# Optimization experiments

Hardware: AMD Instinct MI355X
Metric: run time of the kernel (lower is better)

Reference implementation:

```python
import jax, jax.numpy as jnp
import numpy as np

N_NODES = 2000
N_EDGES = 40000
DILATION = 2
DC = 32  # dilation_channels
C_IN = 32  # in_channels (= gcn out_channels)


def setup_inputs() -> dict:
    key = jax.random.key(0)
    ks = jax.random.split(key, 8)
    x = jax.random.normal(ks[0], (4, 34, N_NODES, C_IN), jnp.float32)
    edge_index = jax.random.randint(ks[1], (2, N_EDGES), 0, N_NODES, dtype=jnp.int64)
    edge_weight = jax.random.uniform(ks[2], (N_EDGES,), jnp.float32)
    gate1_w = jax.random.normal(ks[3], (DC, C_IN, 1, 2), jnp.float32) * 0.1
    gate1_b = jnp.zeros((DC,), jnp.float32)
    gate2_w = jax.random.normal(ks[4], (DC, C_IN, 1, 2), jnp.float32) * 0.1
    gate2_b = jnp.zeros((DC,), jnp.float32)
    gcn_w = jax.random.normal(ks[5], (DC, C_IN), jnp.float32) * 0.1
    gcn_b = jnp.zeros((C_IN,), jnp.float32)
    return {"x": x, "edge_index": edge_index, "edge_weight": edge_weight,
            "gate1_w": gate1_w, "gate1_b": gate1_b,
            "gate2_w": gate2_w, "gate2_b": gate2_b,
            "gcn_w": gcn_w, "gcn_b": gcn_b}


def _gate_conv(x_nchw, w, b):
    # Conv2d(kernel=(1,2), dilation=DILATION), VALID padding -> acts on time (W) axis
    y = jax.lax.conv_general_dilated(
        x_nchw, w, window_strides=(1, 1), padding='VALID',
        rhs_dilation=(1, DILATION),
        dimension_numbers=('NCHW', 'OIHW', 'NCHW'))
    return y + b[None, :, None, None]


def reference(x, edge_index, edge_weight, gate1_w, gate1_b, gate2_w, gate2_b, gcn_w, gcn_b):
    B, T, N, C = x.shape
    xt = jnp.transpose(x, (0, 3, 2, 1))  # (B, C, N, T)
    g1 = jnp.tanh(_gate_conv(xt, gate1_w, gate1_b))      # (B, DC, N, T')
    g2 = jax.nn.sigmoid(_gate_conv(xt, gate2_w, gate2_b))
    g = g1 * g2
    Tp = g.shape[-1]
    h = jnp.transpose(g, (0, 3, 2, 1)).reshape(B * Tp, N, DC)  # (Bt, N, DC)

    # GCN normalization with self loops (PyG gcn_norm, add_self_loops=True)
    row, col = edge_index[0], edge_index[1]
    loop = jnp.arange(N, dtype=edge_index.dtype)
    row_f = jnp.concatenate([row, loop])
    col_f = jnp.concatenate([col, loop])
    w_f = jnp.concatenate([edge_weight, jnp.ones((N,), edge_weight.dtype)])
    deg = jax.ops.segment_sum(w_f, col_f, num_segments=N)
    dis = jnp.where(deg > 0, jax.lax.rsqrt(deg), 0.0)
    norm = dis[row_f] * w_f * dis[col_f]  # (E+N,)

    hw = jnp.einsum('bnd,de->bne', h, gcn_w)          # (Bt, N, C_IN)
    msgs = hw[:, row_f, :] * norm[None, :, None]      # (Bt, E+N, C_IN)
    out = jnp.zeros_like(hw).at[:, col_f, :].add(msgs) + gcn_b  # scatter over targets

    return out.reshape(B, Tp, N, C_IN)  # (B, T', N, in_channels)
```

## Files before the change

### kernel.cpp

```cpp
#include <hip/hip_runtime.h>
#include <hip/hip_bf16.h>

typedef short short8 __attribute__((ext_vector_type(8)));
typedef float floatx4 __attribute__((ext_vector_type(4)));
typedef unsigned short ushort8_t __attribute__((ext_vector_type(8)));

#define NN 2000
#define NE 40000
#define NB 4
#define T_IN 34
#define TP 32
#define NBT (NB * TP)
#define NPOS (NB * TP * NN)
#define CAP 96


__device__ inline unsigned short f2bf(float x) {
    unsigned int u = __float_as_uint(x);
    u = u + 0x7fff + ((u >> 16) & 1);
    return (unsigned short)(u >> 16);
}
__device__ inline void splitPair(float x0, float x1, unsigned& hi, unsigned& lo) {
    unsigned u0 = __float_as_uint(x0), u1 = __float_as_uint(x1);
    hi = __builtin_amdgcn_perm(u1, u0, 0x07060302u);
    float r0 = x0 - __uint_as_float(u0 & 0xffff0000u);
    float r1 = x1 - __uint_as_float(u1 & 0xffff0000u);
    lo = __builtin_amdgcn_perm(__float_as_uint(r1), __float_as_uint(r0), 0x07060302u);
}
__device__ inline void splitA8(const float* v, short8& hi, short8& lo) {
    union { unsigned u[4]; short8 s; } H, L;
#pragma unroll
    for (int j = 0; j < 4; ++j) {
        unsigned h_, l_;
        splitPair(v[2 * j], v[2 * j + 1], h_, l_);
        H.u[j] = h_; L.u[j] = l_;
    }
    hi = H.s; lo = L.s;
}

__global__ __launch_bounds__(256) void conv_deg_kernel(
        const float* __restrict__ x,
        const float* __restrict__ w1, const float* __restrict__ b1,
        const float* __restrict__ w2, const float* __restrict__ b2,
        unsigned short* __restrict__ h2,
        const int* __restrict__ row, const int* __restrict__ col,
        const float* __restrict__ ew,
        float* __restrict__ deg, int* __restrict__ cursor,
        int2* __restrict__ pcsr) {
    if (blockIdx.x >= 1000) {
        int e = (blockIdx.x - 1000) * 256 + threadIdx.x;
        if (e < NE) {
            int c = col[e], r = row[e];
            float w = ew[e];
            atomicAdd(&deg[c], w);
            int slot = atomicAdd(&cursor[c], 1);
            if (slot < CAP) pcsr[c * CAP + slot] = make_int2(r, __float_as_int(w));
        }
        return;
    }

    int l = threadIdx.x & 63;
    int w = threadIdx.x >> 6;
    int colL = l & 15, q = l >> 4;

    short8 Whi[2][2][2], Wlo[2][2][2];
#pragma unroll
    for (int g = 0; g < 2; ++g) {
        const float* wp = g ? w2 : w1;
#pragma unroll
        for (int d = 0; d < 2; ++d)
#pragma unroll
        for (int tap = 0; tap < 2; ++tap) {
            float wv[8];
#pragma unroll
            for (int j = 0; j < 8; ++j)
                wv[j] = wp[(d * 16 + colL) * 64 + (q * 8 + j) * 2 + tap];
            splitA8(wv, Whi[g][d][tap], Wlo[g][d][tap]);
        }
    }
    float bias[2][2] = { { b1[colL], b1[colL + 16] }, { b2[colL], b2[colL + 16] } };

    for (int i = 0; i < 4; ++i) {
        int tile = blockIdx.x * 16 + w * 4 + i;
        int pos0 = tile * 16;
        int bt = pos0 / 2000;
        int n0 = pos0 - bt * 2000;
        int b_ = bt >> 5, t_ = bt & 31;
        const float* xa = x + (((b_ * T_IN + t_) * NN) + n0 + colL) * 32 + q * 8;
        const float* xb = xa + 2 * NN * 32;
        float va[8], vb[8];
        *(float4*)va       = *(const float4*)xa;
        *(float4*)(va + 4) = *(const float4*)(xa + 4);
        *(float4*)vb       = *(const float4*)xb;
        *(float4*)(vb + 4) = *(const float4*)(xb + 4);
        short8 Ahi0, Alo0, Ahi1, Alo1;
        splitA8(va, Ahi0, Alo0);
        splitA8(vb, Ahi1, Alo1);

        floatx4 acc[2][2];
#pragma unroll
        for (int g = 0; g < 2; ++g)
#pragma unroll
        for (int d = 0; d < 2; ++d) {
            float bv = bias[g][d];
            floatx4 a = { bv, bv, bv, bv };
            a = __builtin_amdgcn_mfma_f32_16x16x32_bf16(Ahi0, Whi[g][d][0], a, 0, 0, 0);
            a = __builtin_amdgcn_mfma_f32_16x16x32_bf16(Ahi1, Whi[g][d][1], a, 0, 0, 0);
            a = __builtin_amdgcn_mfma_f32_16x16x32_bf16(Alo0, Whi[g][d][0], a, 0, 0, 0);
            a = __builtin_amdgcn_mfma_f32_16x16x32_bf16(Alo1, Whi[g][d][1], a, 0, 0, 0);
            a = __builtin_amdgcn_mfma_f32_16x16x32_bf16(Ahi0, Wlo[g][d][0], a, 0, 0, 0);
            a = __builtin_amdgcn_mfma_f32_16x16x32_bf16(Ahi1, Wlo[g][d][1], a, 0, 0, 0);
            acc[g][d] = a;
        }

#pragma unroll
        for (int d = 0; d < 2; ++d)
#pragma unroll
        for (int r = 0; r < 4; ++r) {
            float g1 = acc[0][d][r];
            float g2 = acc[1][d][r];
            float e2 = __expf(2.0f * g1);
            float th = (e2 - 1.0f) / (e2 + 1.0f);
            float sg = 1.0f / (1.0f + __expf(-g2));
            float h = th * sg;
            int n = n0 + q * 4 + r;
            h2[(n * NBT + bt) * 32 + d * 16 + colL] = f2bf(h);
        }
    }
}

__device__ inline void acc8(float2* a2, const ushort8_t& v, float nr) {
    union { ushort8_t s; unsigned u[4]; } U; U.s = v;
#pragma unroll
    for (int j = 0; j < 4; ++j) {
        float2 vv;
        vv.x = __uint_as_float(U.u[j] << 16);
        vv.y = __uint_as_float(U.u[j] & 0xffff0000u);
        a2[j].x += vv.x * nr;
        a2[j].y += vv.y * nr;
    }
}

__global__ __launch_bounds__(256) void agg_gcn_kernel(
        const unsigned short* __restrict__ h2,
        const float* __restrict__ deg, const int* __restrict__ cursor,
        const int2* __restrict__ pcsr,
        const float* __restrict__ gw, const float* __restrict__ gb,
        float* __restrict__ out) {
    __shared__ float st[64 * 36];
    int l = threadIdx.x & 63;
    int wv = threadIdx.x >> 6;
    int b = blockIdx.x;
    int cp = b & 7;
    int n = (b >> 3) * 4 + wv;
    int colL = l & 15, q = l >> 4;

    short8 Bhi[2], Blo[2];
#pragma unroll
    for (int d = 0; d < 2; ++d) {
        float wv8[8];
#pragma unroll
        for (int j = 0; j < 8; ++j)
            wv8[j] = gw[(q * 8 + j) * 32 + d * 16 + colL];
        splitA8(wv8, Bhi[d], Blo[d]);
    }
    float gb0 = gb[colL], gb1 = gb[colL + 16];

    const unsigned short* base = h2 + cp * 512 + l * 8;
    float dn = rsqrtf(deg[n] + 1.0f);
    float w0 = dn * dn;
    float2 a2[4] = { {0,0}, {0,0}, {0,0}, {0,0} };
    {
        ushort8_t sv = *(const ushort8_t*)(base + (size_t)n * 4096);
        acc8(a2, sv, w0);
    }
    int cnt = cursor[n]; if (cnt > CAP) cnt = CAP;
    const int2* slots = pcsr + n * CAP;
    int i = 0;
    for (; i + 8 <= cnt; i += 8) {
        int2 e0 = slots[i],     e1 = slots[i + 1], e2 = slots[i + 2], e3 = slots[i + 3];
        int2 e4 = slots[i + 4], e5 = slots[i + 5], e6 = slots[i + 6], e7 = slots[i + 7];
        float n0 = rsqrtf(deg[e0.x] + 1.0f) * __int_as_float(e0.y) * dn;
        float n1 = rsqrtf(deg[e1.x] + 1.0f) * __int_as_float(e1.y) * dn;
        float n2 = rsqrtf(deg[e2.x] + 1.0f) * __int_as_float(e2.y) * dn;
        float n3 = rsqrtf(deg[e3.x] + 1.0f) * __int_as_float(e3.y) * dn;
        float n4 = rsqrtf(deg[e4.x] + 1.0f) * __int_as_float(e4.y) * dn;
        float n5 = rsqrtf(deg[e5.x] + 1.0f) * __int_as_float(e5.y) * dn;
        float n6 = rsqrtf(deg[e6.x] + 1.0f) * __int_as_float(e6.y) * dn;
        float n7 = rsqrtf(deg[e7.x] + 1.0f) * __int_as_float(e7.y) * dn;
        ushort8_t v0 = *(const ushort8_t*)(base + (size_t)e0.x * 4096);
        ushort8_t v1 = *(const ushort8_t*)(base + (size_t)e1.x * 4096);
        ushort8_t v2 = *(const ushort8_t*)(base + (size_t)e2.x * 4096);
        ushort8_t v3 = *(const ushort8_t*)(base + (size_t)e3.x * 4096);
        ushort8_t v4 = *(const ushort8_t*)(base + (size_t)e4.x * 4096);
        ushort8_t v5 = *(const ushort8_t*)(base + (size_t)e5.x * 4096);
        ushort8_t v6 = *(const ushort8_t*)(base + (size_t)e6.x * 4096);
        ushort8_t v7 = *(const ushort8_t*)(base + (size_t)e7.x * 4096);
        acc8(a2, v0, n0); acc8(a2, v1, n1); acc8(a2, v2, n2); acc8(a2, v3, n3);
        acc8(a2, v4, n4); acc8(a2, v5, n5); acc8(a2, v6, n6); acc8(a2, v7, n7);
    }
    for (; i + 4 <= cnt; i += 4) {
        int2 e0 = slots[i], e1 = slots[i + 1], e2 = slots[i + 2], e3 = slots[i + 3];
        float n0 = rsqrtf(deg[e0.x] + 1.0f) * __int_as_float(e0.y) * dn;
        float n1 = rsqrtf(deg[e1.x] + 1.0f) * __int_as_float(e1.y) * dn;
        float n2 = rsqrtf(deg[e2.x] + 1.0f) * __int_as_float(e2.y) * dn;
        float n3 = rsqrtf(deg[e3.x] + 1.0f) * __int_as_float(e3.y) * dn;
        ushort8_t v0 = *(const ushort8_t*)(base + (size_t)e0.x * 4096);
        ushort8_t v1 = *(const ushort8_t*)(base + (size_t)e1.x * 4096);
        ushort8_t v2 = *(const ushort8_t*)(base + (size_t)e2.x * 4096);
        ushort8_t v3 = *(const ushort8_t*)(base + (size_t)e3.x * 4096);
        acc8(a2, v0, n0); acc8(a2, v1, n1); acc8(a2, v2, n2); acc8(a2, v3, n3);
    }
    for (; i < cnt; ++i) {
        int2 e0 = slots[i];
        float n0 = rsqrtf(deg[e0.x] + 1.0f) * __int_as_float(e0.y) * dn;
        ushort8_t v0 = *(const ushort8_t*)(base + (size_t)e0.x * 4096);
        acc8(a2, v0, n0);
    }

    float* dst = &st[(wv * 16 + (l >> 2)) * 36 + (l & 3) * 8];
    *(float4*)dst       = make_float4(a2[0].x, a2[0].y, a2[1].x, a2[1].y);
    *(float4*)(dst + 4) = make_float4(a2[2].x, a2[2].y, a2[3].x, a2[3].y);
    __syncthreads();

    float av[8];
    const float* ap = &st[(wv * 16 + colL) * 36 + q * 8];
    *(float4*)av       = *(const float4*)ap;
    *(float4*)(av + 4) = *(const float4*)(ap + 4);
    short8 Ahi, Alo;
    splitA8(av, Ahi, Alo);
    floatx4 z = { 0.f, 0.f, 0.f, 0.f };
    floatx4 acc0 = z, acc1 = z;
    acc0 = __builtin_amdgcn_mfma_f32_16x16x32_bf16(Ahi, Bhi[0], acc0, 0, 0, 0);
    acc0 = __builtin_amdgcn_mfma_f32_16x16x32_bf16(Alo, Bhi[0], acc0, 0, 0, 0);
    acc0 = __builtin_amdgcn_mfma_f32_16x16x32_bf16(Ahi, Blo[0], acc0, 0, 0, 0);
    acc1 = __builtin_amdgcn_mfma_f32_16x16x32_bf16(Ahi, Bhi[1], acc1, 0, 0, 0);
    acc1 = __builtin_amdgcn_mfma_f32_16x16x32_bf16(Alo, Bhi[1], acc1, 0, 0, 0);
    acc1 = __builtin_amdgcn_mfma_f32_16x16x32_bf16(Ahi, Blo[1], acc1, 0, 0, 0);
#pragma unroll
    for (int r = 0; r < 4; ++r) {
        int btl = q * 4 + r;
        size_t o = ((size_t)(cp * 16 + btl) * NN + n) << 5;
        out[o + colL]      = acc0[r] + gb0;
        out[o + colL + 16] = acc1[r] + gb1;
    }
}

extern "C" void kernel_launch(void* const* d_in, const int* in_sizes, int n_in,
                              void* d_out, int out_size, void* d_ws, size_t ws_size,
                              hipStream_t stream) {
    const float* x   = (const float*)d_in[0];
    const int*   ei  = (const int*)d_in[1];
    const float* ew  = (const float*)d_in[2];
    const float* g1w = (const float*)d_in[3];
    const float* g1b = (const float*)d_in[4];
    const float* g2w = (const float*)d_in[5];
    const float* g2b = (const float*)d_in[6];
    const float* gcw = (const float*)d_in[7];
    const float* gcb = (const float*)d_in[8];
    float* out = (float*)d_out;

    float* wsf      = (float*)d_ws;
    float* deg      = wsf;
    int*   cursor   = (int*)(wsf + 2048);
    int2*  pcsr     = (int2*)(wsf + 4096);
    unsigned short* h2 = (unsigned short*)(wsf + 388096);

    const int* row = ei;
    const int* col = ei + NE;

    hipMemsetAsync(wsf, 0, 4096 * sizeof(float), stream);
    hipLaunchKernelGGL(conv_deg_kernel, dim3(1157), dim3(256), 0, stream,
                       x, g1w, g1b, g2w, g2b, h2, row, col, ew,
                       deg, cursor, pcsr);
    hipLaunchKernelGGL(agg_gcn_kernel, dim3(4000), dim3(256), 0, stream,
                       h2, deg, cursor, pcsr, gcw, gcb, out);
}
```

Before: 147.7 us.

## Split each node's edge gathering across two waves and schedule edge blocks first

In the aggregation kernel, each node's incoming edges are now split between two wavefronts that take interleaved edge slots. The two partial sums are combined through shared memory before the MFMA projection, and the grid doubles to 8000 blocks. In the conv kernel, the edge-scatter blocks move to the lowest block indices so they are dispatched first. The intent is more memory parallelism for the latency-bound gathers. The cost is half the waves idling during the MFMA stage, more blocks overall, and a shorter unroll per wave.

Measured after the change: 151.6 us. +2.6%, slower.

```diff
diff --git a/kernel.cpp b/kernel.cpp
--- a/kernel.cpp
+++ b/kernel.cpp
@@ -13,6 +13,7 @@
 #define NBT (NB * TP)
 #define NPOS (NB * TP * NN)
 #define CAP 96
+#define NEB 157
 
 
 __device__ inline unsigned short f2bf(float x) {
@@ -47,8 +48,8 @@
         const float* __restrict__ ew,
         float* __restrict__ deg, int* __restrict__ cursor,
         int2* __restrict__ pcsr) {
-    if (blockIdx.x >= 1000) {
-        int e = (blockIdx.x - 1000) * 256 + threadIdx.x;
+    if (blockIdx.x < NEB) {
+        int e = blockIdx.x * 256 + threadIdx.x;
         if (e < NE) {
             int c = col[e], r = row[e];
             float w = ew[e];
@@ -81,7 +82,7 @@
     float bias[2][2] = { { b1[colL], b1[colL + 16] }, { b2[colL], b2[colL + 16] } };
 
     for (int i = 0; i < 4; ++i) {
-        int tile = blockIdx.x * 16 + w * 4 + i;
+        int tile = (blockIdx.x - NEB) * 16 + w * 4 + i;
         int pos0 = tile * 16;
         int bt = pos0 / 2000;
         int n0 = pos0 - bt * 2000;
@@ -152,7 +153,8 @@
     int wv = threadIdx.x >> 6;
     int b = blockIdx.x;
     int cp = b & 7;
-    int n = (b >> 3) * 4 + wv;
+    int n = (b >> 3) * 2 + (wv >> 1);
+    int hf = wv & 1;
     int colL = l & 15, q = l >> 4;
 
     short8 Bhi[2], Blo[2];
@@ -168,39 +170,16 @@
 
     const unsigned short* base = h2 + cp * 512 + l * 8;
     float dn = rsqrtf(deg[n] + 1.0f);
-    float w0 = dn * dn;
     float2 a2[4] = { {0,0}, {0,0}, {0,0}, {0,0} };
-    {
+    if (hf == 0) {
         ushort8_t sv = *(const ushort8_t*)(base + (size_t)n * 4096);
-        acc8(a2, sv, w0);
+        acc8(a2, sv, dn * dn);
     }
     int cnt = cursor[n]; if (cnt > CAP) cnt = CAP;
     const int2* slots = pcsr + n * CAP;
-    int i = 0;
-    for (; i + 8 <= cnt; i += 8) {
-        int2 e0 = slots[i],     e1 = slots[i + 1], e2 = slots[i + 2], e3 = slots[i + 3];
-        int2 e4 = slots[i + 4], e5 = slots[i + 5], e6 = slots[i + 6], e7 = slots[i + 7];
-        float n0 = rsqrtf(deg[e0.x] + 1.0f) * __int_as_float(e0.y) * dn;
-        float n1 = rsqrtf(deg[e1.x] + 1.0f) * __int_as_float(e1.y) * dn;
-        float n2 = rsqrtf(deg[e2.x] + 1.0f) * __int_as_float(e2.y) * dn;
-        float n3 = rsqrtf(deg[e3.x] + 1.0f) * __int_as_float(e3.y) * dn;
-        float n4 = rsqrtf(deg[e4.x] + 1.0f) * __int_as_float(e4.y) * dn;
-        float n5 = rsqrtf(deg[e5.x] + 1.0f) * __int_as_float(e5.y) * dn;
-        float n6 = rsqrtf(deg[e6.x] + 1.0f) * __int_as_float(e6.y) * dn;
-        float n7 = rsqrtf(deg[e7.x] + 1.0f) * __int_as_float(e7.y) * dn;
-        ushort8_t v0 = *(const ushort8_t*)(base + (size_t)e0.x * 4096);
-        ushort8_t v1 = *(const ushort8_t*)(base + (size_t)e1.x * 4096);
-        ushort8_t v2 = *(const ushort8_t*)(base + (size_t)e2.x * 4096);
-        ushort8_t v3 = *(const ushort8_t*)(base + (size_t)e3.x * 4096);
-        ushort8_t v4 = *(const ushort8_t*)(base + (size_t)e4.x * 4096);
-        ushort8_t v5 = *(const ushort8_t*)(base + (size_t)e5.x * 4096);
-        ushort8_t v6 = *(const ushort8_t*)(base + (size_t)e6.x * 4096);
-        ushort8_t v7 = *(const ushort8_t*)(base + (size_t)e7.x * 4096);
-        acc8(a2, v0, n0); acc8(a2, v1, n1); acc8(a2, v2, n2); acc8(a2, v3, n3);
-        acc8(a2, v4, n4); acc8(a2, v5, n5); acc8(a2, v6, n6); acc8(a2, v7, n7);
-    }
-    for (; i + 4 <= cnt; i += 4) {
-        int2 e0 = slots[i], e1 = slots[i + 1], e2 = slots[i + 2], e3 = slots[i + 3];
+    int i = hf;
+    for (; i + 6 < cnt; i += 8) {
+        int2 e0 = slots[i], e1 = slots[i + 2], e2 = slots[i + 4], e3 = slots[i + 6];
         float n0 = rsqrtf(deg[e0.x] + 1.0f) * __int_as_float(e0.y) * dn;
         float n1 = rsqrtf(deg[e1.x] + 1.0f) * __int_as_float(e1.y) * dn;
         float n2 = rsqrtf(deg[e2.x] + 1.0f) * __int_as_float(e2.y) * dn;
@@ -211,7 +190,7 @@
         ushort8_t v3 = *(const ushort8_t*)(base + (size_t)e3.x * 4096);
         acc8(a2, v0, n0); acc8(a2, v1, n1); acc8(a2, v2, n2); acc8(a2, v3, n3);
     }
-    for (; i < cnt; ++i) {
+    for (; i < cnt; i += 2) {
         int2 e0 = slots[i];
         float n0 = rsqrtf(deg[e0.x] + 1.0f) * __int_as_float(e0.y) * dn;
         ushort8_t v0 = *(const ushort8_t*)(base + (size_t)e0.x * 4096);
@@ -223,26 +202,31 @@
     *(float4*)(dst + 4) = make_float4(a2[2].x, a2[2].y, a2[3].x, a2[3].y);
     __syncthreads();
 
-    float av[8];
-    const float* ap = &st[(wv * 16 + colL) * 36 + q * 8];
-    *(float4*)av       = *(const float4*)ap;
-    *(float4*)(av + 4) = *(const float4*)(ap + 4);
-    short8 Ahi, Alo;
-    splitA8(av, Ahi, Alo);
-    floatx4 z = { 0.f, 0.f, 0.f, 0.f };
-    floatx4 acc0 = z, acc1 = z;
-    acc0 = __builtin_amdgcn_mfma_f32_16x16x32_bf16(Ahi, Bhi[0], acc0, 0, 0, 0);
-    acc0 = __builtin_amdgcn_mfma_f32_16x16x32_bf16(Alo, Bhi[0], acc0, 0, 0, 0);
-    acc0 = __builtin_amdgcn_mfma_f32_16x16x32_bf16(Ahi, Blo[0], acc0, 0, 0, 0);
-    acc1 = __builtin_amdgcn_mfma_f32_16x16x32_bf16(Ahi, Bhi[1], acc1, 0, 0, 0);
-    acc1 = __builtin_amdgcn_mfma_f32_16x16x32_bf16(Alo, Bhi[1], acc1, 0, 0, 0);
-    acc1 = __builtin_amdgcn_mfma_f32_16x16x32_bf16(Ahi, Blo[1], acc1, 0, 0, 0);
-#pragma unroll
-    for (int r = 0; r < 4; ++r) {
-        int btl = q * 4 + r;
-        size_t o = ((size_t)(cp * 16 + btl) * NN + n) << 5;
-        out[o + colL]      = acc0[r] + gb0;
-        out[o + colL + 16] = acc1[r] + gb1;
+    if (hf == 0) {
+        float av[8];
+        const float* ap0 = &st[(wv * 16 + colL) * 36 + q * 8];
+        const float* ap1 = ap0 + 16 * 36;
+        float4 x0 = *(const float4*)ap0, x1 = *(const float4*)(ap0 + 4);
+        float4 y0 = *(const float4*)ap1, y1 = *(const float4*)(ap1 + 4);
+        av[0] = x0.x + y0.x; av[1] = x0.y + y0.y; av[2] = x0.z + y0.z; av[3] = x0.w + y0.w;
+        av[4] = x1.x + y1.x; av[5] = x1.y + y1.y; av[6] = x1.z + y1.z; av[7] = x1.w + y1.w;
+        short8 Ahi, Alo;
+        splitA8(av, Ahi, Alo);
+        floatx4 z = { 0.f, 0.f, 0.f, 0.f };
+        floatx4 acc0 = z, acc1 = z;
+        acc0 = __builtin_amdgcn_mfma_f32_16x16x32_bf16(Ahi, Bhi[0], acc0, 0, 0, 0);
+        acc0 = __builtin_amdgcn_mfma_f32_16x16x32_bf16(Alo, Bhi[0], acc0, 0, 0, 0);
+        acc0 = __builtin_amdgcn_mfma_f32_16x16x32_bf16(Ahi, Blo[0], acc0, 0, 0, 0);
+        acc1 = __builtin_amdgcn_mfma_f32_16x16x32_bf16(Ahi, Bhi[1], acc1, 0, 0, 0);
+        acc1 = __builtin_amdgcn_mfma_f32_16x16x32_bf16(Alo, Bhi[1], acc1, 0, 0, 0);
+        acc1 = __builtin_amdgcn_mfma_f32_16x16x32_bf16(Ahi, Blo[1], acc1, 0, 0, 0);
+#pragma unroll
+        for (int r = 0; r < 4; ++r) {
+            int btl = q * 4 + r;
+            size_t o = ((size_t)(cp * 16 + btl) * NN + n) << 5;
+            out[o + colL]      = acc0[r] + gb0;
+            out[o + colL + 16] = acc1[r] + gb1;
+        }
     }
 }
 
@@ -270,9 +254,9 @@
     const int* col = ei + NE;
 
     hipMemsetAsync(wsf, 0, 4096 * sizeof(float), stream);
-    hipLaunchKernelGGL(conv_deg_kernel, dim3(1157), dim3(256), 0, stream,
+    hipLaunchKernelGGL(conv_deg_kernel, dim3(NEB + 1000), dim3(256), 0, stream,
                        x, g1w, g1b, g2w, g2b, h2, row, col, ew,
                        deg, cursor, pcsr);
-    hipLaunchKernelGGL(agg_gcn_kernel, dim3(4000), dim3(256), 0, stream,
+    hipLaunchKernelGGL(agg_gcn_kernel, dim3(8000), dim3(256), 0, stream,
                        h2, deg, cursor, pcsr, gcw, gcb, out);
 }
```
